# Optimization experiments

Measured on AMD Instinct MI355X. Metric: run time of the kernel, lower is better.

Reference implementation:

```python
import jax, jax.numpy as jnp
from jax import lax
import numpy as np

IN, HID, OUT = 28, 64, 10


def _lstm_layer(x_seq, W_ih, W_hh, b_ih, b_hh):
    # x_seq: [B, T, in]; PyTorch gate order: i, f, g, o (stacked along 4H)
    B = x_seq.shape[0]
    H = W_hh.shape[1]
    # Precompute input projection for all timesteps: [B, T, 4H]
    x_proj = jnp.einsum('bti,gi->btg', x_seq, W_ih) + b_ih + b_hh

    def step(carry, xt):
        h, c = carry
        gates = xt + h @ W_hh.T  # [B, 4H]
        i, f, g, o = jnp.split(gates, 4, axis=-1)
        i = jax.nn.sigmoid(i)
        f = jax.nn.sigmoid(f)
        g = jnp.tanh(g)
        o = jax.nn.sigmoid(o)
        c = f * c + i * g
        h = o * jnp.tanh(c)
        return (h, c), h

    h0 = jnp.zeros((B, H), x_seq.dtype)
    (_, _), hs = lax.scan(step, (h0, h0), jnp.swapaxes(x_proj, 0, 1))
    return jnp.swapaxes(hs, 0, 1)  # [B, T, H]


def setup_inputs() -> dict:
    key = jax.random.key(0)
    ks = jax.random.split(key, 12)
    s_in = 1.0 / np.sqrt(HID)
    u = lambda k, shape: jax.random.uniform(k, shape, jnp.float32, -s_in, s_in)
    return {
        'x': jax.random.normal(ks[0], (16384, 1, 28, 28), jnp.float32),
        'W_ih0': u(ks[1], (4 * HID, IN)),
        'W_hh0': u(ks[2], (4 * HID, HID)),
        'b_ih0': u(ks[3], (4 * HID,)),
        'b_hh0': u(ks[4], (4 * HID,)),
        'W_ih1': u(ks[5], (4 * HID, HID)),
        'W_hh1': u(ks[6], (4 * HID, HID)),
        'b_ih1': u(ks[7], (4 * HID,)),
        'b_hh1': u(ks[8], (4 * HID,)),
        'W_lin': u(ks[9], (OUT, HID)),
        'b_lin': u(ks[10], (OUT,)),
    }


def reference(x, W_ih0, W_hh0, b_ih0, b_hh0, W_ih1, W_hh1, b_ih1, b_hh1, W_lin, b_lin):
    # (N, C, H, W) -> (N, C*H, W): sequence of rows, feature = W = 28
    x = x.reshape(x.shape[0], -1, x.shape[-1])
    h1 = _lstm_layer(x, W_ih0, W_hh0, b_ih0, b_hh0)   # [B, T, 64]
    h2 = _lstm_layer(h1, W_ih1, W_hh1, b_ih1, b_hh1)  # [B, T, 64]
    last = h2[:, -1, :]
    return last @ W_lin.T + b_lin  # [B, 10]
```

## Files before the change

### kernel.cpp

```cpp
#include <hip/hip_runtime.h>


typedef _Float16 half8 __attribute__((ext_vector_type(8)));
typedef float floatx4 __attribute__((ext_vector_type(4)));

__device__ __forceinline__ void gate_batch4(const floatx4 (&acc)[2][2], float (&c)[4],
                                            _Float16* __restrict__ plane,
                                            const int (&hwr)[2][2]) {
    float ei[4], ef[4], eg[4], eo[4];
    #pragma unroll
    for (int tt = 0; tt < 4; ++tt) {
        floatx4 a = acc[tt >> 1][tt & 1];
        ei[tt] = __expf(-a[0]);
        ef[tt] = __expf(-a[1]);
        eg[tt] = __expf(2.0f * a[2]);
        eo[tt] = __expf(-a[3]);
    }
    float ri[4], rf[4], rg[4], ro[4];
    #pragma unroll
    for (int tt = 0; tt < 4; ++tt) {
        ri[tt] = __builtin_amdgcn_rcpf(1.0f + ei[tt]);
        rf[tt] = __builtin_amdgcn_rcpf(1.0f + ef[tt]);
        rg[tt] = __builtin_amdgcn_rcpf(1.0f + eg[tt]);
        ro[tt] = __builtin_amdgcn_rcpf(1.0f + eo[tt]);
    }
    float ec[4];
    #pragma unroll
    for (int tt = 0; tt < 4; ++tt) {
        float tg = 1.0f - 2.0f * rg[tt];
        float cn = rf[tt] * c[tt] + ri[tt] * tg;
        c[tt] = cn;
        ec[tt] = __expf(2.0f * cn);
    }
    #pragma unroll
    for (int tt = 0; tt < 4; ++tt) {
        float tc = 1.0f - 2.0f * __builtin_amdgcn_rcpf(ec[tt] + 1.0f);
        plane[hwr[tt >> 1][tt & 1]] = (_Float16)(ro[tt] * tc);
    }
}

__launch_bounds__(512, 2)
__global__ void lstm_mfma(const float* __restrict__ x,
                          const float* __restrict__ Wih0, const float* __restrict__ Whh0,
                          const float* __restrict__ bih0, const float* __restrict__ bhh0,
                          const float* __restrict__ Wih1, const float* __restrict__ Whh1,
                          const float* __restrict__ bih1, const float* __restrict__ bhh1,
                          const float* __restrict__ Wlin, const float* __restrict__ blin,
                          float* __restrict__ out) {
    __shared__ __align__(16) _Float16 h0p[2][2048];
    __shared__ __align__(16) _Float16 h1p[2][2048];
    __shared__ __align__(16) _Float16 xb[2][1024];
    __shared__ float wlin_s[640];
    __shared__ float blin_s[10];

    const int lane = threadIdx.x;
    const int w    = threadIdx.y;
    const int tid  = w * 64 + lane;
    const int quad = lane >> 4;
    const int col  = lane & 15;

    half8 A0[2][3], A1[2][4];
    #pragma unroll
    for (int im = 0; im < 2; ++im) {
        int mt = 2 * w + im;
        int m  = mt * 16 + col;
        int u  = m >> 2, g = m & 3;
        int row = g * 64 + u;
        #pragma unroll
        for (int kt = 0; kt < 3; ++kt) {
            half8 r;
            #pragma unroll
            for (int j = 0; j < 8; ++j) {
                int k = kt * 32 + quad * 8 + j;
                float v;
                if (k < 28)       v = Wih0[row * 28 + k];
                else if (k == 28) v = bih0[row] + bhh0[row];
                else if (k < 32)  v = 0.f;
                else              v = Whh0[row * 64 + (k - 32)];
                r[j] = (_Float16)v;
            }
            A0[im][kt] = r;
        }
        #pragma unroll
        for (int kt = 0; kt < 4; ++kt) {
            half8 r;
            #pragma unroll
            for (int j = 0; j < 8; ++j) {
                int k = kt * 32 + quad * 8 + j;
                float v = (k < 64) ? Wih1[row * 64 + k] : Whh1[row * 64 + (k - 64)];
                r[j] = (_Float16)v;
            }
            A1[im][kt] = r;
        }
    }
    floatx4 bias1[2];
    #pragma unroll
    for (int im = 0; im < 2; ++im) {
        int u = (2 * w + im) * 4 + quad;
        #pragma unroll
        for (int r = 0; r < 4; ++r) bias1[im][r] = bih1[r * 64 + u] + bhh1[r * 64 + u];
    }

    int xrd[2], hrd[2][2], hwr[2][2];
    #pragma unroll
    for (int in = 0; in < 2; ++in) {
        xrd[in] = in * 512 + lane * 8;
        #pragma unroll
        for (int kt = 0; kt < 2; ++kt) hrd[kt][in] = (in * 2 + kt) * 512 + lane * 8;
        #pragma unroll
        for (int im = 0; im < 2; ++im) {
            int u = (2 * w + im) * 4 + quad;
            hwr[im][in] = (in * 2 + (u >> 5)) * 512 + (((u >> 3) & 3) * 16 + col) * 8 + (u & 7);
        }
    }

    const int xi = tid & 31;
    const bool xvalid = xi < 28;
    const float* xg[2];
    int xstg[2];
    #pragma unroll
    for (int s = 0; s < 2; ++s) {
        int b = (tid >> 5) + s * 16;
        xg[s]   = x + (blockIdx.x * 32 + b) * 784 + xi;
        xstg[s] = (b >> 4) * 512 + ((xi >> 3) * 16 + (b & 15)) * 8 + (xi & 7);
    }

    {
        int* z0 = (int*)&h0p[1][0];
        int* z1 = (int*)&h1p[1][0];
        #pragma unroll
        for (int i = tid; i < 1024; i += 512) { z0[i] = 0; z1[i] = 0; }
        #pragma unroll
        for (int s = 0; s < 2; ++s) {
            float xv = xvalid ? xg[s][0] : 0.f;
            xb[0][xstg[s]] = (xi == 28) ? (_Float16)1.0f : (_Float16)xv;
        }
    }
    __syncthreads();

    float c0[4] = {0.f, 0.f, 0.f, 0.f};
    float c1[4] = {0.f, 0.f, 0.f, 0.f};

    {
        float xn[2] = {0.f, 0.f};
        #pragma unroll
        for (int s = 0; s < 2; ++s)
            if (xvalid) xn[s] = xg[s][28];

        floatx4 acc0[2][2];
        #pragma unroll
        for (int im = 0; im < 2; ++im)
            #pragma unroll
            for (int in = 0; in < 2; ++in)
                acc0[im][in] = (floatx4){0.f, 0.f, 0.f, 0.f};
        #pragma unroll
        for (int in = 0; in < 2; ++in) {
            half8 bf = *(const half8*)&xb[0][xrd[in]];
            #pragma unroll
            for (int im = 0; im < 2; ++im)
                acc0[im][in] = __builtin_amdgcn_mfma_f32_16x16x32_f16(A0[im][0], bf, acc0[im][in], 0, 0, 0);
        }
        #pragma unroll
        for (int kt = 0; kt < 2; ++kt) {
            #pragma unroll
            for (int in = 0; in < 2; ++in) {
                half8 bf = *(const half8*)&h0p[1][hrd[kt][in]];
                #pragma unroll
                for (int im = 0; im < 2; ++im)
                    acc0[im][in] = __builtin_amdgcn_mfma_f32_16x16x32_f16(A0[im][kt + 1], bf, acc0[im][in], 0, 0, 0);
            }
        }
        gate_batch4(acc0, c0, &h0p[0][0], hwr);
        #pragma unroll
        for (int s = 0; s < 2; ++s)
            xb[1][xstg[s]] = (xi == 28) ? (_Float16)1.0f : (_Float16)xn[s];
        __syncthreads();
    }

    for (int p = 0; p < 27; ++p) {
        const int pr  = p & 1;
        const int pr1 = pr ^ 1;
        const _Float16* h0r = &h0p[pr][0];
        _Float16*       h0w = &h0p[pr1][0];
        const _Float16* h1r = &h1p[pr1][0];
        _Float16*       h1w = &h1p[pr][0];
        const _Float16* xr  = &xb[pr1][0];
        _Float16*       xw  = &xb[pr][0];

        const int xoff = (p < 26 ? p + 2 : 27) * 28;
        float xn[2] = {0.f, 0.f};
        #pragma unroll
        for (int s = 0; s < 2; ++s)
            if (xvalid) xn[s] = xg[s][xoff];

        half8 bh0[2][2], bh1[2][2], bx[2];
        #pragma unroll
        for (int in = 0; in < 2; ++in) {
            bx[in] = *(const half8*)&xr[xrd[in]];
            #pragma unroll
            for (int kt = 0; kt < 2; ++kt) {
                bh0[kt][in] = *(const half8*)&h0r[hrd[kt][in]];
                bh1[kt][in] = *(const half8*)&h1r[hrd[kt][in]];
            }
        }

        floatx4 acc0[2][2], acc1[2][2];
        #pragma unroll
        for (int im = 0; im < 2; ++im)
            #pragma unroll
            for (int in = 0; in < 2; ++in) {
                acc0[im][in] = (floatx4){0.f, 0.f, 0.f, 0.f};
                acc1[im][in] = bias1[im];
            }
        #pragma unroll
        for (int in = 0; in < 2; ++in)
            #pragma unroll
            for (int im = 0; im < 2; ++im)
                acc0[im][in] = __builtin_amdgcn_mfma_f32_16x16x32_f16(A0[im][0], bx[in], acc0[im][in], 0, 0, 0);
        #pragma unroll
        for (int kt = 0; kt < 2; ++kt)
            #pragma unroll
            for (int in = 0; in < 2; ++in)
                #pragma unroll
                for (int im = 0; im < 2; ++im) {
                    acc0[im][in] = __builtin_amdgcn_mfma_f32_16x16x32_f16(A0[im][kt + 1], bh0[kt][in], acc0[im][in], 0, 0, 0);
                    acc1[im][in] = __builtin_amdgcn_mfma_f32_16x16x32_f16(A1[im][kt],     bh0[kt][in], acc1[im][in], 0, 0, 0);
                    acc1[im][in] = __builtin_amdgcn_mfma_f32_16x16x32_f16(A1[im][kt + 2], bh1[kt][in], acc1[im][in], 0, 0, 0);
                }

        gate_batch4(acc0, c0, h0w, hwr);
        gate_batch4(acc1, c1, h1w, hwr);
        #pragma unroll
        for (int s = 0; s < 2; ++s)
            xw[xstg[s]] = (xi == 28) ? (_Float16)1.0f : (_Float16)xn[s];
        __syncthreads();
    }

    {
        floatx4 acc1[2][2];
        #pragma unroll
        for (int im = 0; im < 2; ++im)
            #pragma unroll
            for (int in = 0; in < 2; ++in)
                acc1[im][in] = bias1[im];
        #pragma unroll
        for (int kt = 0; kt < 2; ++kt) {
            #pragma unroll
            for (int in = 0; in < 2; ++in) {
                half8 b0 = *(const half8*)&h0p[1][hrd[kt][in]];
                half8 b1 = *(const half8*)&h1p[0][hrd[kt][in]];
                #pragma unroll
                for (int im = 0; im < 2; ++im) {
                    acc1[im][in] = __builtin_amdgcn_mfma_f32_16x16x32_f16(A1[im][kt],     b0, acc1[im][in], 0, 0, 0);
                    acc1[im][in] = __builtin_amdgcn_mfma_f32_16x16x32_f16(A1[im][kt + 2], b1, acc1[im][in], 0, 0, 0);
                }
            }
        }
        gate_batch4(acc1, c1, &h1p[1][0], hwr);
        __syncthreads();
    }

    #pragma unroll
    for (int i = tid; i < 640; i += 512) wlin_s[i] = Wlin[i];
    if (tid < 10) blin_s[tid] = blin[tid];
    __syncthreads();
    if (tid < 320) {
        int b = tid / 10, o = tid - b * 10;
        float a = blin_s[o];
        #pragma unroll 8
        for (int u = 0; u < 64; ++u) {
            float hv = (float)h1p[1][((b >> 4) * 2 + (u >> 5)) * 512 + (((u >> 3) & 3) * 16 + (b & 15)) * 8 + (u & 7)];
            a += wlin_s[o * 64 + u] * hv;
        }
        out[(blockIdx.x * 32 + b) * 10 + o] = a;
    }
}

extern "C" void kernel_launch(void* const* d_in, const int* in_sizes, int n_in,
                              void* d_out, int out_size, void* d_ws, size_t ws_size,
                              hipStream_t stream) {
    const float* x    = (const float*)d_in[0];
    const float* Wih0 = (const float*)d_in[1];
    const float* Whh0 = (const float*)d_in[2];
    const float* bih0 = (const float*)d_in[3];
    const float* bhh0 = (const float*)d_in[4];
    const float* Wih1 = (const float*)d_in[5];
    const float* Whh1 = (const float*)d_in[6];
    const float* bih1 = (const float*)d_in[7];
    const float* bhh1 = (const float*)d_in[8];
    const float* Wlin = (const float*)d_in[9];
    const float* blin = (const float*)d_in[10];
    float* out = (float*)d_out;

    lstm_mfma<<<512, dim3(64, 8), 0, stream>>>(x, Wih0, Whh0, bih0, bhh0,
                                               Wih1, Whh1, bih1, bhh1, Wlin, blin, out);
}
```

Baseline: 209.2 us.

## Unroll interior timestep loop by two with compile-time buffer parity, raise occupancy hint

After: 213.8 us. 1.02x slower.

```diff
diff --git a/kernel.cpp b/kernel.cpp
--- a/kernel.cpp
+++ b/kernel.cpp
@@ -39,7 +39,77 @@
     }
 }
 
-__launch_bounds__(512, 2)
+template <int PR>
+__device__ __forceinline__ void interior_phase(
+        int xoff, const float* const (&xg)[2], bool xvalid, int xi, const int (&xstg)[2],
+        const half8 (&A0)[2][3], const half8 (&A1)[2][4], const floatx4 (&bias1)[2],
+        float (&c0)[4], float (&c1)[4],
+        const int (&xrd)[2], const int (&hrd)[2][2], const int (&hwr)[2][2],
+        _Float16* __restrict__ h0p, _Float16* __restrict__ h1p, _Float16* __restrict__ xb) {
+    constexpr int H0R = PR * 2048, H0W = (PR ^ 1) * 2048;
+    constexpr int H1R = (PR ^ 1) * 2048, H1W = PR * 2048;
+    constexpr int XR = (PR ^ 1) * 1024, XW = PR * 1024;
+
+    float xn[2] = {0.f, 0.f};
+    #pragma unroll
+    for (int s = 0; s < 2; ++s)
+        if (xvalid) xn[s] = xg[s][xoff];
+
+    half8 bx[2], bh0[2][2];
+    #pragma unroll
+    for (int in = 0; in < 2; ++in) {
+        bx[in] = *(const half8*)&xb[XR + xrd[in]];
+        #pragma unroll
+        for (int kt = 0; kt < 2; ++kt)
+            bh0[kt][in] = *(const half8*)&h0p[H0R + hrd[kt][in]];
+    }
+
+    floatx4 acc0[2][2], acc1[2][2];
+    #pragma unroll
+    for (int im = 0; im < 2; ++im)
+        #pragma unroll
+        for (int in = 0; in < 2; ++in) {
+            acc0[im][in] = (floatx4){0.f, 0.f, 0.f, 0.f};
+            acc1[im][in] = bias1[im];
+        }
+    #pragma unroll
+    for (int in = 0; in < 2; ++in)
+        #pragma unroll
+        for (int im = 0; im < 2; ++im)
+            acc0[im][in] = __builtin_amdgcn_mfma_f32_16x16x32_f16(A0[im][0], bx[in], acc0[im][in], 0, 0, 0);
+    #pragma unroll
+    for (int kt = 0; kt < 2; ++kt)
+        #pragma unroll
+        for (int in = 0; in < 2; ++in)
+            #pragma unroll
+            for (int im = 0; im < 2; ++im) {
+                acc0[im][in] = __builtin_amdgcn_mfma_f32_16x16x32_f16(A0[im][kt + 1], bh0[kt][in], acc0[im][in], 0, 0, 0);
+                acc1[im][in] = __builtin_amdgcn_mfma_f32_16x16x32_f16(A1[im][kt],     bh0[kt][in], acc1[im][in], 0, 0, 0);
+            }
+    half8 bh1[2][2];
+    #pragma unroll
+    for (int kt = 0; kt < 2; ++kt)
+        #pragma unroll
+        for (int in = 0; in < 2; ++in)
+            bh1[kt][in] = *(const half8*)&h1p[H1R + hrd[kt][in]];
+    #pragma unroll
+    for (int kt = 0; kt < 2; ++kt)
+        #pragma unroll
+        for (int in = 0; in < 2; ++in)
+            #pragma unroll
+            for (int im = 0; im < 2; ++im)
+                acc1[im][in] = __builtin_amdgcn_mfma_f32_16x16x32_f16(A1[im][kt + 2], bh1[kt][in], acc1[im][in], 0, 0, 0);
+
+    gate_batch4(acc0, c0, &h0p[H0W], hwr);
+    gate_batch4(acc1, c1, &h1p[H1W], hwr);
+
+    #pragma unroll
+    for (int s = 0; s < 2; ++s)
+        xb[XW + xstg[s]] = (xi == 28) ? (_Float16)1.0f : (_Float16)xn[s];
+    __syncthreads();
+}
+
+__launch_bounds__(512, 4)
 __global__ void lstm_mfma(const float* __restrict__ x,
                           const float* __restrict__ Wih0, const float* __restrict__ Whh0,
                           const float* __restrict__ bih0, const float* __restrict__ bhh0,
@@ -47,9 +117,9 @@
                           const float* __restrict__ bih1, const float* __restrict__ bhh1,
                           const float* __restrict__ Wlin, const float* __restrict__ blin,
                           float* __restrict__ out) {
-    __shared__ __align__(16) _Float16 h0p[2][2048];
-    __shared__ __align__(16) _Float16 h1p[2][2048];
-    __shared__ __align__(16) _Float16 xb[2][1024];
+    __shared__ __align__(16) _Float16 h0p[2 * 2048];
+    __shared__ __align__(16) _Float16 h1p[2 * 2048];
+    __shared__ __align__(16) _Float16 xb[2 * 1024];
     __shared__ float wlin_s[640];
     __shared__ float blin_s[10];
 
@@ -126,14 +196,14 @@
     }
 
     {
-        int* z0 = (int*)&h0p[1][0];
-        int* z1 = (int*)&h1p[1][0];
+        int* z0 = (int*)&h0p[2048];
+        int* z1 = (int*)&h1p[2048];
         #pragma unroll
         for (int i = tid; i < 1024; i += 512) { z0[i] = 0; z1[i] = 0; }
         #pragma unroll
         for (int s = 0; s < 2; ++s) {
             float xv = xvalid ? xg[s][0] : 0.f;
-            xb[0][xstg[s]] = (xi == 28) ? (_Float16)1.0f : (_Float16)xv;
+            xb[xstg[s]] = (xi == 28) ? (_Float16)1.0f : (_Float16)xv;
         }
     }
     __syncthreads();
@@ -155,7 +225,7 @@
                 acc0[im][in] = (floatx4){0.f, 0.f, 0.f, 0.f};
         #pragma unroll
         for (int in = 0; in < 2; ++in) {
-            half8 bf = *(const half8*)&xb[0][xrd[in]];
+            half8 bf = *(const half8*)&xb[xrd[in]];
             #pragma unroll
             for (int im = 0; im < 2; ++im)
                 acc0[im][in] = __builtin_amdgcn_mfma_f32_16x16x32_f16(A0[im][0], bf, acc0[im][in], 0, 0, 0);
@@ -164,77 +234,30 @@
         for (int kt = 0; kt < 2; ++kt) {
             #pragma unroll
             for (int in = 0; in < 2; ++in) {
-                half8 bf = *(const half8*)&h0p[1][hrd[kt][in]];
+                half8 bf = *(const half8*)&h0p[2048 + hrd[kt][in]];
                 #pragma unroll
                 for (int im = 0; im < 2; ++im)
                     acc0[im][in] = __builtin_amdgcn_mfma_f32_16x16x32_f16(A0[im][kt + 1], bf, acc0[im][in], 0, 0, 0);
             }
         }
-        gate_batch4(acc0, c0, &h0p[0][0], hwr);
+        gate_batch4(acc0, c0, &h0p[0], hwr);
         #pragma unroll
         for (int s = 0; s < 2; ++s)
-            xb[1][xstg[s]] = (xi == 28) ? (_Float16)1.0f : (_Float16)xn[s];
+            xb[1024 + xstg[s]] = (xi == 28) ? (_Float16)1.0f : (_Float16)xn[s];
         __syncthreads();
     }
 
-    for (int p = 0; p < 27; ++p) {
-        const int pr  = p & 1;
-        const int pr1 = pr ^ 1;
-        const _Float16* h0r = &h0p[pr][0];
-        _Float16*       h0w = &h0p[pr1][0];
-        const _Float16* h1r = &h1p[pr1][0];
-        _Float16*       h1w = &h1p[pr][0];
-        const _Float16* xr  = &xb[pr1][0];
-        _Float16*       xw  = &xb[pr][0];
-
-        const int xoff = (p < 26 ? p + 2 : 27) * 28;
-        float xn[2] = {0.f, 0.f};
-        #pragma unroll
-        for (int s = 0; s < 2; ++s)
-            if (xvalid) xn[s] = xg[s][xoff];
-
-        half8 bh0[2][2], bh1[2][2], bx[2];
-        #pragma unroll
-        for (int in = 0; in < 2; ++in) {
-            bx[in] = *(const half8*)&xr[xrd[in]];
-            #pragma unroll
-            for (int kt = 0; kt < 2; ++kt) {
-                bh0[kt][in] = *(const half8*)&h0r[hrd[kt][in]];
-                bh1[kt][in] = *(const half8*)&h1r[hrd[kt][in]];
-            }
-        }
-
-        floatx4 acc0[2][2], acc1[2][2];
-        #pragma unroll
-        for (int im = 0; im < 2; ++im)
-            #pragma unroll
-            for (int in = 0; in < 2; ++in) {
-                acc0[im][in] = (floatx4){0.f, 0.f, 0.f, 0.f};
-                acc1[im][in] = bias1[im];
-            }
-        #pragma unroll
-        for (int in = 0; in < 2; ++in)
-            #pragma unroll
-            for (int im = 0; im < 2; ++im)
-                acc0[im][in] = __builtin_amdgcn_mfma_f32_16x16x32_f16(A0[im][0], bx[in], acc0[im][in], 0, 0, 0);
-        #pragma unroll
-        for (int kt = 0; kt < 2; ++kt)
-            #pragma unroll
-            for (int in = 0; in < 2; ++in)
-                #pragma unroll
-                for (int im = 0; im < 2; ++im) {
-                    acc0[im][in] = __builtin_amdgcn_mfma_f32_16x16x32_f16(A0[im][kt + 1], bh0[kt][in], acc0[im][in], 0, 0, 0);
-                    acc1[im][in] = __builtin_amdgcn_mfma_f32_16x16x32_f16(A1[im][kt],     bh0[kt][in], acc1[im][in], 0, 0, 0);
-                    acc1[im][in] = __builtin_amdgcn_mfma_f32_16x16x32_f16(A1[im][kt + 2], bh1[kt][in], acc1[im][in], 0, 0, 0);
-                }
-
-        gate_batch4(acc0, c0, h0w, hwr);
-        gate_batch4(acc1, c1, h1w, hwr);
-        #pragma unroll
-        for (int s = 0; s < 2; ++s)
-            xw[xstg[s]] = (xi == 28) ? (_Float16)1.0f : (_Float16)xn[s];
-        __syncthreads();
-    }
+    int xoff = 2 * 28;
+    #pragma unroll 1
+    for (int pp = 0; pp < 13; ++pp) {
+        interior_phase<0>(xoff,      xg, xvalid, xi, xstg, A0, A1, bias1, c0, c1,
+                          xrd, hrd, hwr, h0p, h1p, xb);
+        interior_phase<1>(xoff + 28, xg, xvalid, xi, xstg, A0, A1, bias1, c0, c1,
+                          xrd, hrd, hwr, h0p, h1p, xb);
+        xoff += 56;
+    }
+    interior_phase<0>(27 * 28, xg, xvalid, xi, xstg, A0, A1, bias1, c0, c1,
+                      xrd, hrd, hwr, h0p, h1p, xb);
 
     {
         floatx4 acc1[2][2];
@@ -247,8 +270,8 @@
         for (int kt = 0; kt < 2; ++kt) {
             #pragma unroll
             for (int in = 0; in < 2; ++in) {
-                half8 b0 = *(const half8*)&h0p[1][hrd[kt][in]];
-                half8 b1 = *(const half8*)&h1p[0][hrd[kt][in]];
+                half8 b0 = *(const half8*)&h0p[2048 + hrd[kt][in]];
+                half8 b1 = *(const half8*)&h1p[hrd[kt][in]];
                 #pragma unroll
                 for (int im = 0; im < 2; ++im) {
                     acc1[im][in] = __builtin_amdgcn_mfma_f32_16x16x32_f16(A1[im][kt],     b0, acc1[im][in], 0, 0, 0);
@@ -256,7 +279,7 @@
                 }
             }
         }
-        gate_batch4(acc1, c1, &h1p[1][0], hwr);
+        gate_batch4(acc1, c1, &h1p[2048], hwr);
         __syncthreads();
     }
 
@@ -269,7 +292,7 @@
         float a = blin_s[o];
         #pragma unroll 8
         for (int u = 0; u < 64; ++u) {
-            float hv = (float)h1p[1][((b >> 4) * 2 + (u >> 5)) * 512 + (((u >> 3) & 3) * 16 + (b & 15)) * 8 + (u & 7)];
+            float hv = (float)h1p[2048 + ((b >> 4) * 2 + (u >> 5)) * 512 + (((u >> 3) & 3) * 16 + (b & 15)) * 8 + (u & 7)];
             a += wlin_s[o * 64 + u] * hv;
         }
         out[(blockIdx.x * 32 + b) * 10 + o] = a;
```
